# Performance work log

Hardware: AMD Instinct MI355X
Metric: run time of the kernel (lower is better)

## Reference

```python
import jax, jax.numpy as jnp
import numpy as np

B, CIN, COUT, H, W = 16, 64, 64, 128, 128
MH, MW = 32, 32  # retained Fourier modes


def setup_inputs() -> dict:
    key = jax.random.key(0)
    k1, k2, k3 = jax.random.split(key, 3)
    scale = 1.0 / (CIN * COUT)  # 'auto' scale in the torch module
    x = jax.random.normal(k1, (B, CIN, H, W), dtype=jnp.float32)
    # packed complex weight: dim0 = (real, imag), dim1 = corner (top=0, bottom=1)
    weight = scale * jax.random.normal(k2, (2, 2, CIN, COUT, MH, MW), dtype=jnp.float32)
    bias = scale * jax.random.normal(k3, (COUT, 1, 1), dtype=jnp.float32)
    return {"x": x, "weight": weight, "bias": bias, "super_res": 1}


def reference(x, weight, bias, super_res):
    b, ci, h, w = x.shape
    # rfft2 over the last two spatial dims (norm='backward' is default)
    xf = jnp.fft.rfft2(x.astype(jnp.float32), norm="backward")  # [b, ci, h, w//2+1] c64
    wc = (weight[0] + 1j * weight[1]).astype(jnp.complex64)  # [2, ci, co, mh, mw]
    # low-frequency corner contractions: bixy,ioxy->boxy
    top = jnp.einsum("bixy,ioxy->boxy", xf[:, :, :MH, :MW], wc[0])
    bot = jnp.einsum("bixy,ioxy->boxy", xf[:, :, h - MH:, :MW], wc[1])
    out_fft = jnp.zeros((b, COUT, h, w // 2 + 1), dtype=jnp.complex64)
    out_fft = out_fft.at[:, :, :MH, :MW:super_res].set(top)
    out_fft = out_fft.at[:, :, h - MH:, :MW:super_res].set(bot)
    out_size = (int(h * super_res), int(w * super_res))
    y = jnp.fft.irfft2(out_fft, s=out_size, norm="backward").astype(x.dtype)
    return y + bias  # bias [co,1,1] broadcasts over spatial dims
```

## Files before the change

### kernel.cpp

```cpp
#include <hip/hip_runtime.h>


__device__ __forceinline__ void build_tab(float* tabs) {
    int t = threadIdx.x;
    if (t < 128) {
        float ang = (float)t * 0.049087385212340517f;
        float s, c;
        sincosf(ang, &s, &c);
        tabs[t] = c;
        tabs[129 + t] = s;
    }
}

__global__ __launch_bounds__(256) void kAB(const float* __restrict__ x,
                                           float* __restrict__ XF) {
    __shared__ float tabs[258];
    __shared__ __align__(16) float smem[8704];
    build_tab(tabs);
    __syncthreads();
    int t = threadIdx.x;
    size_t bc = blockIdx.x;
    float* Twid = smem;
    float* xeo  = smem + 4096;
    #pragma unroll
    for (int i = 0; i < 16; ++i) {
        int e = t + i * 256;
        int w = e >> 6, q = e & 63, kx = q >> 1;
        int idx = (w * kx) & 127;
        Twid[e] = (q & 1) ? -tabs[129 + idx] : tabs[idx];
    }
    const float* xb = x + bc * 16384;
    int th = t & 31;
    int tq = t >> 5;
    int q0 = tq * 8;
    int wl4 = (t & 3) * 4;
    int hb  = t >> 2;
    float4 rlo0, rhi0, rlo1, rhi1;
    auto loadR = [&](int ph) {
        rlo0 = *(const float4*)(xb + hb * 128 + ph * 16 + wl4);
        rhi0 = *(const float4*)(xb + hb * 128 + ph * 16 + wl4 + 64);
        rlo1 = *(const float4*)(xb + (64 + hb) * 128 + ph * 16 + wl4);
        rhi1 = *(const float4*)(xb + (64 + hb) * 128 + ph * 16 + wl4 + 64);
    };
    auto writeR = [&]() {
        int h0 = hb, h1 = 64 + hb;
        *(float2*)(&xeo[(wl4+0)*260 + 2*h0]) = make_float2(rlo0.x+rhi0.x, rlo0.x-rhi0.x);
        *(float2*)(&xeo[(wl4+1)*260 + 2*h0]) = make_float2(rlo0.y+rhi0.y, rlo0.y-rhi0.y);
        *(float2*)(&xeo[(wl4+2)*260 + 2*h0]) = make_float2(rlo0.z+rhi0.z, rlo0.z-rhi0.z);
        *(float2*)(&xeo[(wl4+3)*260 + 2*h0]) = make_float2(rlo0.w+rhi0.w, rlo0.w-rhi0.w);
        *(float2*)(&xeo[(wl4+0)*260 + 2*h1]) = make_float2(rlo1.x+rhi1.x, rlo1.x-rhi1.x);
        *(float2*)(&xeo[(wl4+1)*260 + 2*h1]) = make_float2(rlo1.y+rhi1.y, rlo1.y-rhi1.y);
        *(float2*)(&xeo[(wl4+2)*260 + 2*h1]) = make_float2(rlo1.z+rhi1.z, rlo1.z-rhi1.z);
        *(float2*)(&xeo[(wl4+3)*260 + 2*h1]) = make_float2(rlo1.w+rhi1.w, rlo1.w-rhi1.w);
    };
    loadR(0);
    writeR();
    float4 acc[8];
    #pragma unroll
    for (int j = 0; j < 8; ++j) acc[j] = make_float4(0.f, 0.f, 0.f, 0.f);
    __syncthreads();
    for (int ph = 0; ph < 4; ++ph) {
        if (ph < 3) loadR(ph + 1);
        #pragma unroll 4
        for (int wl = 0; wl < 16; ++wl) {
            int w = ph * 16 + wl;
            const float* xr = &xeo[wl * 260 + 4 * th];
            float4 d0  = *(const float4*)(xr);
            float4 d1  = *(const float4*)(xr + 128);
            float4 tw0 = *(const float4*)(&Twid[w * 64 + q0]);
            float4 tw1 = *(const float4*)(&Twid[w * 64 + q0 + 4]);
            acc[0].x = fmaf(d0.x, tw0.x, acc[0].x); acc[0].y = fmaf(d0.x, tw0.y, acc[0].y);
            acc[0].z = fmaf(d0.y, tw0.z, acc[0].z); acc[0].w = fmaf(d0.y, tw0.w, acc[0].w);
            acc[1].x = fmaf(d0.x, tw1.x, acc[1].x); acc[1].y = fmaf(d0.x, tw1.y, acc[1].y);
            acc[1].z = fmaf(d0.y, tw1.z, acc[1].z); acc[1].w = fmaf(d0.y, tw1.w, acc[1].w);
            acc[2].x = fmaf(d0.z, tw0.x, acc[2].x); acc[2].y = fmaf(d0.z, tw0.y, acc[2].y);
            acc[2].z = fmaf(d0.w, tw0.z, acc[2].z); acc[2].w = fmaf(d0.w, tw0.w, acc[2].w);
            acc[3].x = fmaf(d0.z, tw1.x, acc[3].x); acc[3].y = fmaf(d0.z, tw1.y, acc[3].y);
            acc[3].z = fmaf(d0.w, tw1.z, acc[3].z); acc[3].w = fmaf(d0.w, tw1.w, acc[3].w);
            acc[4].x = fmaf(d1.x, tw0.x, acc[4].x); acc[4].y = fmaf(d1.x, tw0.y, acc[4].y);
            acc[4].z = fmaf(d1.y, tw0.z, acc[4].z); acc[4].w = fmaf(d1.y, tw0.w, acc[4].w);
            acc[5].x = fmaf(d1.x, tw1.x, acc[5].x); acc[5].y = fmaf(d1.x, tw1.y, acc[5].y);
            acc[5].z = fmaf(d1.y, tw1.z, acc[5].z); acc[5].w = fmaf(d1.y, tw1.w, acc[5].w);
            acc[6].x = fmaf(d1.z, tw0.x, acc[6].x); acc[6].y = fmaf(d1.z, tw0.y, acc[6].y);
            acc[6].z = fmaf(d1.w, tw0.z, acc[6].z); acc[6].w = fmaf(d1.w, tw0.w, acc[6].w);
            acc[7].x = fmaf(d1.z, tw1.x, acc[7].x); acc[7].y = fmaf(d1.z, tw1.y, acc[7].y);
            acc[7].z = fmaf(d1.w, tw1.z, acc[7].z); acc[7].w = fmaf(d1.w, tw1.w, acc[7].w);
        }
        __syncthreads();
        if (ph < 3) {
            writeR();
            __syncthreads();
        }
    }
    float* Af = smem;
    {
        int base = th * 68 + q0;
        *(float4*)(&Af[base])          = make_float4(acc[0].x+acc[4].x, acc[0].y+acc[4].y, acc[0].z+acc[4].z, acc[0].w+acc[4].w);
        *(float4*)(&Af[base + 4])      = make_float4(acc[1].x+acc[5].x, acc[1].y+acc[5].y, acc[1].z+acc[5].z, acc[1].w+acc[5].w);
        *(float4*)(&Af[2176 + base])   = make_float4(acc[0].x-acc[4].x, acc[0].y-acc[4].y, acc[0].z-acc[4].z, acc[0].w-acc[4].w);
        *(float4*)(&Af[2176 + base+4]) = make_float4(acc[1].x-acc[5].x, acc[1].y-acc[5].y, acc[1].z-acc[5].z, acc[1].w-acc[5].w);
        *(float4*)(&Af[4352 + base])   = make_float4(acc[2].x+acc[6].x, acc[2].y+acc[6].y, acc[2].z+acc[6].z, acc[2].w+acc[6].w);
        *(float4*)(&Af[4352 + base+4]) = make_float4(acc[3].x+acc[7].x, acc[3].y+acc[7].y, acc[3].z+acc[7].z, acc[3].w+acc[7].w);
        *(float4*)(&Af[6528 + base])   = make_float4(acc[2].x-acc[6].x, acc[2].y-acc[6].y, acc[2].z-acc[6].z, acc[2].w-acc[6].w);
        *(float4*)(&Af[6528 + base+4]) = make_float4(acc[3].x-acc[7].x, acc[3].y-acc[7].y, acc[3].z-acc[7].z, acc[3].w-acc[7].w);
    }
    __syncthreads();
    {
        int k = t & 31, kxg = t >> 5;
        int kx0 = kxg * 4;
        int sig = k & 1;
        const float* pe = Af + sig * 2176;
        const float* po = Af + 4352 + sig * 2176;
        int a2 = (2 * k) & 127;
        float ca = tabs[a2], sa = tabs[129 + a2];
        float ce = 1.f, se = 0.f;
        float co_ = tabs[k], so_ = tabs[129 + k];
        float4 P1 = {0,0,0,0}, P2 = {0,0,0,0}, P3 = {0,0,0,0}, P4 = {0,0,0,0};
        for (int m = 0; m < 32; ++m) {
            float4 ae01 = *(const float4*)(pe + m * 68 + 2 * kx0);
            float4 ae23 = *(const float4*)(pe + m * 68 + 2 * kx0 + 4);
            float4 ao01 = *(const float4*)(po + m * 68 + 2 * kx0);
            float4 ao23 = *(const float4*)(po + m * 68 + 2 * kx0 + 4);
            P1.x = fmaf(ae01.x, ce, P1.x); P1.x = fmaf(ao01.x, co_, P1.x);
            P2.x = fmaf(ae01.y, se, P2.x); P2.x = fmaf(ao01.y, so_, P2.x);
            P3.x = fmaf(ae01.y, ce, P3.x); P3.x = fmaf(ao01.y, co_, P3.x);
            P4.x = fmaf(ae01.x, se, P4.x); P4.x = fmaf(ao01.x, so_, P4.x);
            P1.y = fmaf(ae01.z, ce, P1.y); P1.y = fmaf(ao01.z, co_, P1.y);
            P2.y = fmaf(ae01.w, se, P2.y); P2.y = fmaf(ao01.w, so_, P2.y);
            P3.y = fmaf(ae01.w, ce, P3.y); P3.y = fmaf(ao01.w, co_, P3.y);
            P4.y = fmaf(ae01.z, se, P4.y); P4.y = fmaf(ao01.z, so_, P4.y);
            P1.z = fmaf(ae23.x, ce, P1.z); P1.z = fmaf(ao23.x, co_, P1.z);
            P2.z = fmaf(ae23.y, se, P2.z); P2.z = fmaf(ao23.y, so_, P2.z);
            P3.z = fmaf(ae23.y, ce, P3.z); P3.z = fmaf(ao23.y, co_, P3.z);
            P4.z = fmaf(ae23.x, se, P4.z); P4.z = fmaf(ao23.x, so_, P4.z);
            P1.w = fmaf(ae23.z, ce, P1.w); P1.w = fmaf(ao23.z, co_, P1.w);
            P2.w = fmaf(ae23.w, se, P2.w); P2.w = fmaf(ao23.w, so_, P2.w);
            P3.w = fmaf(ae23.w, ce, P3.w); P3.w = fmaf(ao23.w, co_, P3.w);
            P4.w = fmaf(ae23.z, se, P4.w); P4.w = fmaf(ao23.z, so_, P4.w);
            float t1 = se * sa, t2 = ce * sa;
            float cen = fmaf(ce, ca, -t1);
            float sen = fmaf(se, ca, t2);
            ce = cen; se = sen;
            float t3 = so_ * sa, t4 = co_ * sa;
            float con = fmaf(co_, ca, -t3);
            float son = fmaf(so_, ca, t4);
            co_ = con; so_ = son;
        }
        float* xfb = XF + bc * 4096;
        *(float4*)(xfb + (k * 32 + kx0) * 2) =
            make_float4(P1.x + P2.x, P3.x - P4.x, P1.y + P2.y, P3.y - P4.y);
        *(float4*)(xfb + (k * 32 + kx0) * 2 + 4) =
            make_float4(P1.z + P2.z, P3.z - P4.z, P1.w + P2.w, P3.w - P4.w);
        if (k) {
            *(float4*)(xfb + ((64 - k) * 32 + kx0) * 2) =
                make_float4(P1.x - P2.x, P3.x + P4.x, P1.y - P2.y, P3.y + P4.y);
            *(float4*)(xfb + ((64 - k) * 32 + kx0) * 2 + 4) =
                make_float4(P1.z - P2.z, P3.z + P4.z, P1.w - P2.w, P3.w + P4.w);
        }
        if (t < 32) {
            int kx = t;
            float re = 0.f, im = 0.f;
            #pragma unroll 8
            for (int m = 0; m < 32; ++m) {
                float2 aep = *(const float2*)(&Af[       m * 68 + 2 * kx]);
                float2 aop = *(const float2*)(&Af[4352 + m * 68 + 2 * kx]);
                float sg = (m & 1) ? -1.f : 1.f;
                re = fmaf(sg, aep.x - aop.y, re);
                im = fmaf(sg, aep.y + aop.x, im);
            }
            xfb[(32 * 32 + kx) * 2]     = re;
            xfb[(32 * 32 + kx) * 2 + 1] = im;
        }
    }
}

__global__ __launch_bounds__(256, 4) void kC(const float* __restrict__ XF,
                                             const float* __restrict__ Wgt,
                                             float* __restrict__ YF0,
                                             float* __restrict__ YF1) {
    __shared__ float2 Xs[2048];
    int t = threadIdx.x;
    int bid = blockIdx.x;
    int cih = bid & 1;
    int mxh = (bid >> 1) & 1;
    int cot = (bid >> 2) & 3;
    int my  = (bid >> 4) & 31;
    int c   = bid >> 9;
    int co0 = cot * 16;
    int slotbase = (c * 32 + my) * 32 + mxh * 16;
    int mx = t & 15;
    int co_l = t >> 4;
    int co = co0 + co_l;
    int ci0 = cih * 32;
    float2 acc[16];
    #pragma unroll
    for (int i = 0; i < 16; ++i) acc[i] = make_float2(0.f, 0.f);
    const float* wp = Wgt + (size_t)c * 4194304 + (size_t)my * 32 + mxh * 16 + mx
                          + ((size_t)(ci0 * 64) + co) * 1024;
    float2 rw0[8], rw1[8], rw2[8], rw3[8], rx[8];
    auto loadW = [&](int cc, float2* rw) {
        #pragma unroll
        for (int j = 0; j < 8; ++j) {
            size_t off = (size_t)(cc * 8 + j) * 65536;
            rw[j].x = wp[off];
            rw[j].y = wp[off + 8388608];
        }
    };
    auto loadX = [&](int cc) {
        #pragma unroll
        for (int s = 0; s < 8; ++s) {
            int e = t + s * 256;
            int emx = e & 15, eb = (e >> 4) & 15, eci = e >> 8;
            int ci = ci0 + cc * 8 + eci;
            rx[s] = *(const float2*)(XF + ((size_t)(eb * 64 + ci) * 2048 + slotbase + emx) * 2);
        }
    };
    auto writeX = [&]() {
        #pragma unroll
        for (int s = 0; s < 8; ++s) Xs[t + s * 256] = rx[s];
    };
#define KC_COMPUTE(RW)                                                       \
    {                                                                        \
        _Pragma("unroll")                                                    \
        for (int j = 0; j < 8; ++j) {                                        \
            float2 w = RW[j];                                                \
            _Pragma("unroll")                                                \
            for (int b = 0; b < 16; ++b) {                                   \
                float2 xv = Xs[(j * 16 + b) * 16 + mx];                      \
                acc[b].x = fmaf(xv.x, w.x, acc[b].x);                        \
                acc[b].x = fmaf(-xv.y, w.y, acc[b].x);                       \
                acc[b].y = fmaf(xv.x, w.y, acc[b].y);                        \
                acc[b].y = fmaf(xv.y, w.x, acc[b].y);                        \
            }                                                                \
        }                                                                    \
    }
    loadX(0);
    loadW(0, rw0); loadW(1, rw1); loadW(2, rw2);
    writeX();
    __syncthreads();
    loadX(1);
    loadW(3, rw3);
    KC_COMPUTE(rw0);
    __syncthreads();
    writeX(); __syncthreads();
    loadX(2);
    KC_COMPUTE(rw1);
    __syncthreads();
    writeX(); __syncthreads();
    loadX(3);
    KC_COMPUTE(rw2);
    __syncthreads();
    writeX(); __syncthreads();
    KC_COMPUTE(rw3);
#undef KC_COMPUTE
    float* YF = cih ? YF1 : YF0;
    #pragma unroll
    for (int b = 0; b < 16; ++b) {
        *(float2*)(YF + ((size_t)(b * 64 + co) * 2048 + slotbase + mx) * 2) = acc[b];
    }
}

__global__ __launch_bounds__(256) void kDE(const float* __restrict__ YF0,
                                           const float* __restrict__ YF1,
                                           const float* __restrict__ bias,
                                           float* __restrict__ out) {
    __shared__ float tabs[258];
    __shared__ __align__(16) float Ts[4096];
    __shared__ __align__(16) float U[8448];
    build_tab(tabs);
    __syncthreads();
    int t = threadIdx.x;
    size_t bo = blockIdx.x;
    const float inv = 6.103515625e-05f;
    #pragma unroll
    for (int i = 0; i < 16; ++i) {
        int e = t + i * 256;
        int q = e >> 6, w = e & 63;
        int k = q >> 1;
        int idx = (k * w) & 127;
        float val;
        if (q == 0)      val = inv;
        else if (q == 1) val = 0.f;
        else if (q & 1)  val = -2.f * inv * tabs[129 + idx];
        else             val =  2.f * inv * tabs[idx];
        Ts[e] = val;
    }
    float* Qs = U;
    float* Rs = U + 2112;
    const float* y0 = YF0 + bo * 4096;
    const float* y1 = YF1 + bo * 4096;
    for (int u = t; u < 528; u += 256) {
        int k = u >> 4, kxf = (u & 15) * 4;
        float4 a0 = *(const float4*)(y0 + k * 64 + kxf);
        float4 a1 = *(const float4*)(y1 + k * 64 + kxf);
        float4 a = make_float4(a0.x+a1.x, a0.y+a1.y, a0.z+a1.z, a0.w+a1.w);
        float4 Q, R;
        if (k == 0) { Q = a; R = make_float4(0.f, 0.f, 0.f, 0.f); }
        else if (k == 32) { Q = a; R = make_float4(-a.x, -a.y, -a.z, -a.w); }
        else {
            float4 b0 = *(const float4*)(y0 + (64 - k) * 64 + kxf);
            float4 b1 = *(const float4*)(y1 + (64 - k) * 64 + kxf);
            float4 bb = make_float4(b0.x+b1.x, b0.y+b1.y, b0.z+b1.z, b0.w+b1.w);
            Q = make_float4(a.x+bb.x, a.y+bb.y, a.z+bb.z, a.w+bb.w);
            R = make_float4(a.x-bb.x, a.y-bb.y, a.z-bb.z, a.w-bb.w);
        }
        *(float4*)(&Qs[k * 64 + kxf]) = Q;
        *(float4*)(&Rs[k * 64 + kxf]) = R;
    }
    __syncthreads();
    int hh = t >> 2;
    int kx0 = (t & 3) * 8;
    float4 Ee0 = {0,0,0,0}, Ee1 = {0,0,0,0}, Ee2 = {0,0,0,0}, Ee3 = {0,0,0,0};
    float4 Eo0 = {0,0,0,0}, Eo1 = {0,0,0,0}, Eo2 = {0,0,0,0}, Eo3 = {0,0,0,0};
    int idx = 0;
#define KD_BODY(E0, E1, E2, E3, kk)                                          \
    {                                                                        \
        float c = tabs[idx], s = tabs[129 + idx];                            \
        const float4* Qp = (const float4*)(&Qs[(kk) * 64 + kx0 * 2]);        \
        const float4* Rp = (const float4*)(&Rs[(kk) * 64 + kx0 * 2]);        \
        float4 Qv, Rv;                                                       \
        Qv = Qp[0]; Rv = Rp[0];                                              \
        E0.x = fmaf(c, Qv.x, E0.x); E0.x = fmaf(-s, Rv.y, E0.x);             \
        E0.y = fmaf(c, Qv.y, E0.y); E0.y = fmaf(s, Rv.x, E0.y);              \
        E0.z = fmaf(c, Qv.z, E0.z); E0.z = fmaf(-s, Rv.w, E0.z);             \
        E0.w = fmaf(c, Qv.w, E0.w); E0.w = fmaf(s, Rv.z, E0.w);              \
        Qv = Qp[1]; Rv = Rp[1];                                              \
        E1.x = fmaf(c, Qv.x, E1.x); E1.x = fmaf(-s, Rv.y, E1.x);             \
        E1.y = fmaf(c, Qv.y, E1.y); E1.y = fmaf(s, Rv.x, E1.y);              \
        E1.z = fmaf(c, Qv.z, E1.z); E1.z = fmaf(-s, Rv.w, E1.z);             \
        E1.w = fmaf(c, Qv.w, E1.w); E1.w = fmaf(s, Rv.z, E1.w);              \
        Qv = Qp[2]; Rv = Rp[2];                                              \
        E2.x = fmaf(c, Qv.x, E2.x); E2.x = fmaf(-s, Rv.y, E2.x);             \
        E2.y = fmaf(c, Qv.y, E2.y); E2.y = fmaf(s, Rv.x, E2.y);              \
        E2.z = fmaf(c, Qv.z, E2.z); E2.z = fmaf(-s, Rv.w, E2.z);             \
        E2.w = fmaf(c, Qv.w, E2.w); E2.w = fmaf(s, Rv.z, E2.w);              \
        Qv = Qp[3]; Rv = Rp[3];                                              \
        E3.x = fmaf(c, Qv.x, E3.x); E3.x = fmaf(-s, Rv.y, E3.x);             \
        E3.y = fmaf(c, Qv.y, E3.y); E3.y = fmaf(s, Rv.x, E3.y);              \
        E3.z = fmaf(c, Qv.z, E3.z); E3.z = fmaf(-s, Rv.w, E3.z);             \
        E3.w = fmaf(c, Qv.w, E3.w); E3.w = fmaf(s, Rv.z, E3.w);              \
        idx = (idx + hh) & 127;                                              \
    }
    for (int u = 0; u < 16; ++u) {
        KD_BODY(Ee0, Ee1, Ee2, Ee3, 2 * u);
        KD_BODY(Eo0, Eo1, Eo2, Eo3, 2 * u + 1);
    }
    KD_BODY(Ee0, Ee1, Ee2, Ee3, 32);
#undef KD_BODY
    __syncthreads();
    float* Zt = U;
    {
        float* zr = &Zt[(2 * kx0) * 132 + hh];
        float* zs = zr + 64;
        zr[0*132]  = Ee0.x + Eo0.x;  zs[0*132]  = Ee0.x - Eo0.x;
        zr[1*132]  = Ee0.y + Eo0.y;  zs[1*132]  = Ee0.y - Eo0.y;
        zr[2*132]  = Ee0.z + Eo0.z;  zs[2*132]  = Ee0.z - Eo0.z;
        zr[3*132]  = Ee0.w + Eo0.w;  zs[3*132]  = Ee0.w - Eo0.w;
        zr[4*132]  = Ee1.x + Eo1.x;  zs[4*132]  = Ee1.x - Eo1.x;
        zr[5*132]  = Ee1.y + Eo1.y;  zs[5*132]  = Ee1.y - Eo1.y;
        zr[6*132]  = Ee1.z + Eo1.z;  zs[6*132]  = Ee1.z - Eo1.z;
        zr[7*132]  = Ee1.w + Eo1.w;  zs[7*132]  = Ee1.w - Eo1.w;
        zr[8*132]  = Ee2.x + Eo2.x;  zs[8*132]  = Ee2.x - Eo2.x;
        zr[9*132]  = Ee2.y + Eo2.y;  zs[9*132]  = Ee2.y - Eo2.y;
        zr[10*132] = Ee2.z + Eo2.z;  zs[10*132] = Ee2.z - Eo2.z;
        zr[11*132] = Ee2.w + Eo2.w;  zs[11*132] = Ee2.w - Eo2.w;
        zr[12*132] = Ee3.x + Eo3.x;  zs[12*132] = Ee3.x - Eo3.x;
        zr[13*132] = Ee3.y + Eo3.y;  zs[13*132] = Ee3.y - Eo3.y;
        zr[14*132] = Ee3.z + Eo3.z;  zs[14*132] = Ee3.z - Eo3.z;
        zr[15*132] = Ee3.w + Eo3.w;  zs[15*132] = Ee3.w - Eo3.w;
    }
    __syncthreads();
    int w0 = (t & 31) * 2;
    int h0 = (t >> 5) * 16;
    float2 We[16], Wo[16];
    #pragma unroll
    for (int j = 0; j < 16; ++j) { We[j] = make_float2(0.f, 0.f); Wo[j] = make_float2(0.f, 0.f); }
#define KE_K(E, K)                                                            \
    {                                                                         \
        const float4* zpe = (const float4*)(&Zt[(2*(K)) * 132 + h0]);         \
        const float4* zpo = (const float4*)(&Zt[(2*(K)+1) * 132 + h0]);       \
        float2 twe = *(const float2*)(&Ts[(2*(K)) * 64 + w0]);                \
        float2 two = *(const float2*)(&Ts[(2*(K)+1) * 64 + w0]);              \
        float4 e0 = zpe[0], e1 = zpe[1], e2 = zpe[2], e3 = zpe[3];            \
        float4 o0 = zpo[0], o1 = zpo[1], o2 = zpo[2], o3 = zpo[3];            \
        E[0].x  = fmaf(e0.x, twe.x, E[0].x);  E[0].x  = fmaf(o0.x, two.x, E[0].x);   \
        E[0].y  = fmaf(e0.x, twe.y, E[0].y);  E[0].y  = fmaf(o0.x, two.y, E[0].y);   \
        E[1].x  = fmaf(e0.y, twe.x, E[1].x);  E[1].x  = fmaf(o0.y, two.x, E[1].x);   \
        E[1].y  = fmaf(e0.y, twe.y, E[1].y);  E[1].y  = fmaf(o0.y, two.y, E[1].y);   \
        E[2].x  = fmaf(e0.z, twe.x, E[2].x);  E[2].x  = fmaf(o0.z, two.x, E[2].x);   \
        E[2].y  = fmaf(e0.z, twe.y, E[2].y);  E[2].y  = fmaf(o0.z, two.y, E[2].y);   \
        E[3].x  = fmaf(e0.w, twe.x, E[3].x);  E[3].x  = fmaf(o0.w, two.x, E[3].x);   \
        E[3].y  = fmaf(e0.w, twe.y, E[3].y);  E[3].y  = fmaf(o0.w, two.y, E[3].y);   \
        E[4].x  = fmaf(e1.x, twe.x, E[4].x);  E[4].x  = fmaf(o1.x, two.x, E[4].x);   \
        E[4].y  = fmaf(e1.x, twe.y, E[4].y);  E[4].y  = fmaf(o1.x, two.y, E[4].y);   \
        E[5].x  = fmaf(e1.y, twe.x, E[5].x);  E[5].x  = fmaf(o1.y, two.x, E[5].x);   \
        E[5].y  = fmaf(e1.y, twe.y, E[5].y);  E[5].y  = fmaf(o1.y, two.y, E[5].y);   \
        E[6].x  = fmaf(e1.z, twe.x, E[6].x);  E[6].x  = fmaf(o1.z, two.x, E[6].x);   \
        E[6].y  = fmaf(e1.z, twe.y, E[6].y);  E[6].y  = fmaf(o1.z, two.y, E[6].y);   \
        E[7].x  = fmaf(e1.w, twe.x, E[7].x);  E[7].x  = fmaf(o1.w, two.x, E[7].x);   \
        E[7].y  = fmaf(e1.w, twe.y, E[7].y);  E[7].y  = fmaf(o1.w, two.y, E[7].y);   \
        E[8].x  = fmaf(e2.x, twe.x, E[8].x);  E[8].x  = fmaf(o2.x, two.x, E[8].x);   \
        E[8].y  = fmaf(e2.x, twe.y, E[8].y);  E[8].y  = fmaf(o2.x, two.y, E[8].y);   \
        E[9].x  = fmaf(e2.y, twe.x, E[9].x);  E[9].x  = fmaf(o2.y, two.x, E[9].x);   \
        E[9].y  = fmaf(e2.y, twe.y, E[9].y);  E[9].y  = fmaf(o2.y, two.y, E[9].y);   \
        E[10].x = fmaf(e2.z, twe.x, E[10].x); E[10].x = fmaf(o2.z, two.x, E[10].x);  \
        E[10].y = fmaf(e2.z, twe.y, E[10].y); E[10].y = fmaf(o2.z, two.y, E[10].y);  \
        E[11].x = fmaf(e2.w, twe.x, E[11].x); E[11].x = fmaf(o2.w, two.x, E[11].x);  \
        E[11].y = fmaf(e2.w, twe.y, E[11].y); E[11].y = fmaf(o2.w, two.y, E[11].y);  \
        E[12].x = fmaf(e3.x, twe.x, E[12].x); E[12].x = fmaf(o3.x, two.x, E[12].x);  \
        E[12].y = fmaf(e3.x, twe.y, E[12].y); E[12].y = fmaf(o3.x, two.y, E[12].y);  \
        E[13].x = fmaf(e3.y, twe.x, E[13].x); E[13].x = fmaf(o3.y, two.x, E[13].x);  \
        E[13].y = fmaf(e3.y, twe.y, E[13].y); E[13].y = fmaf(o3.y, two.y, E[13].y);  \
        E[14].x = fmaf(e3.z, twe.x, E[14].x); E[14].x = fmaf(o3.z, two.x, E[14].x);  \
        E[14].y = fmaf(e3.z, twe.y, E[14].y); E[14].y = fmaf(o3.z, two.y, E[14].y);  \
        E[15].x = fmaf(e3.w, twe.x, E[15].x); E[15].x = fmaf(o3.w, two.x, E[15].x);  \
        E[15].y = fmaf(e3.w, twe.y, E[15].y); E[15].y = fmaf(o3.w, two.y, E[15].y);  \
    }
    #pragma unroll 2
    for (int u = 0; u < 16; ++u) {
        KE_K(We, 2 * u);
        KE_K(Wo, 2 * u + 1);
    }
#undef KE_K
    float bv = bias[(int)(bo & 63)];
    float* ob = out + ((size_t)(bo * 128 + h0)) * 128;
    #pragma unroll
    for (int j = 0; j < 16; ++j) {
        float2 lo = make_float2(We[j].x + Wo[j].x + bv, We[j].y + Wo[j].y + bv);
        float2 hi = make_float2(We[j].x - Wo[j].x + bv, We[j].y - Wo[j].y + bv);
        *(float2*)(ob + (size_t)j * 128 + w0)      = lo;
        *(float2*)(ob + (size_t)j * 128 + w0 + 64) = hi;
    }
}

extern "C" void kernel_launch(void* const* d_in, const int* in_sizes, int n_in,
                              void* d_out, int out_size, void* d_ws, size_t ws_size,
                              hipStream_t stream) {
    (void)in_sizes; (void)n_in; (void)out_size; (void)ws_size;
    const float* x    = (const float*)d_in[0];
    const float* wgt  = (const float*)d_in[1];
    const float* bias = (const float*)d_in[2];
    float* outp   = (float*)d_out;
    char* ws = (char*)d_ws;
    float* bufXF  = (float*)(ws + (48u << 20));
    float* bufYF0 = (float*)(ws);
    float* bufYF1 = (float*)(ws + (16u << 20));
    hipLaunchKernelGGL(kAB, dim3(1024), dim3(256), 0, stream, x, bufXF);
    hipLaunchKernelGGL(kC, dim3(1024), dim3(256), 0, stream, bufXF, wgt, bufYF0, bufYF1);
    hipLaunchKernelGGL(kDE, dim3(1024), dim3(256), 0, stream, bufYF0, bufYF1, bias, outp);
}
```

Baseline: 116.9 us.

## Split kC work over batch halves and double-buffer weight registers

The spectral contraction kernel now assigns each block 8 output channels and splits the 16-batch dimension across two thread halves, so each thread keeps 8 accumulators instead of 16. The grid doubles to 2048 blocks. Weight prefetch moves from four register buffers to two ping-pong buffers that are reloaded after each compute stage. This lowers register pressure and adds parallelism, at the cost of loading each X tile in twice as many blocks and exposing more of the weight-load latency.

```diff
diff --git a/kernel.cpp b/kernel.cpp
--- a/kernel.cpp
+++ b/kernel.cpp
@@ -183,21 +183,22 @@
     int bid = blockIdx.x;
     int cih = bid & 1;
     int mxh = (bid >> 1) & 1;
-    int cot = (bid >> 2) & 3;
-    int my  = (bid >> 4) & 31;
-    int c   = bid >> 9;
-    int co0 = cot * 16;
+    int cot = (bid >> 2) & 7;
+    int my  = (bid >> 5) & 31;
+    int c   = bid >> 10;
+    int co0 = cot * 8;
     int slotbase = (c * 32 + my) * 32 + mxh * 16;
-    int mx = t & 15;
-    int co_l = t >> 4;
+    int mx   = t & 15;
+    int co_l = (t >> 4) & 7;
+    int bh   = t >> 7;
     int co = co0 + co_l;
     int ci0 = cih * 32;
-    float2 acc[16];
-    #pragma unroll
-    for (int i = 0; i < 16; ++i) acc[i] = make_float2(0.f, 0.f);
+    float2 acc[8];
+    #pragma unroll
+    for (int i = 0; i < 8; ++i) acc[i] = make_float2(0.f, 0.f);
     const float* wp = Wgt + (size_t)c * 4194304 + (size_t)my * 32 + mxh * 16 + mx
                           + ((size_t)(ci0 * 64) + co) * 1024;
-    float2 rw0[8], rw1[8], rw2[8], rw3[8], rx[8];
+    float2 rwA[8], rwB[8], rx[8];
     auto loadW = [&](int cc, float2* rw) {
         #pragma unroll
         for (int j = 0; j < 8; ++j) {
@@ -225,38 +226,39 @@
         for (int j = 0; j < 8; ++j) {                                        \
             float2 w = RW[j];                                                \
             _Pragma("unroll")                                                \
-            for (int b = 0; b < 16; ++b) {                                   \
-                float2 xv = Xs[(j * 16 + b) * 16 + mx];                      \
-                acc[b].x = fmaf(xv.x, w.x, acc[b].x);                        \
-                acc[b].x = fmaf(-xv.y, w.y, acc[b].x);                       \
-                acc[b].y = fmaf(xv.x, w.y, acc[b].y);                        \
-                acc[b].y = fmaf(xv.y, w.x, acc[b].y);                        \
+            for (int bb = 0; bb < 8; ++bb) {                                 \
+                float2 xv = Xs[(j * 16 + bh * 8 + bb) * 16 + mx];            \
+                acc[bb].x = fmaf(xv.x, w.x, acc[bb].x);                      \
+                acc[bb].x = fmaf(-xv.y, w.y, acc[bb].x);                     \
+                acc[bb].y = fmaf(xv.x, w.y, acc[bb].y);                      \
+                acc[bb].y = fmaf(xv.y, w.x, acc[bb].y);                      \
             }                                                                \
         }                                                                    \
     }
-    loadX(0);
-    loadW(0, rw0); loadW(1, rw1); loadW(2, rw2);
+    loadX(0); loadW(0, rwA); loadW(1, rwB);
     writeX();
     __syncthreads();
     loadX(1);
-    loadW(3, rw3);
-    KC_COMPUTE(rw0);
+    KC_COMPUTE(rwA);
+    loadW(2, rwA);
     __syncthreads();
     writeX(); __syncthreads();
     loadX(2);
-    KC_COMPUTE(rw1);
+    KC_COMPUTE(rwB);
+    loadW(3, rwB);
     __syncthreads();
     writeX(); __syncthreads();
     loadX(3);
-    KC_COMPUTE(rw2);
+    KC_COMPUTE(rwA);
     __syncthreads();
     writeX(); __syncthreads();
-    KC_COMPUTE(rw3);
+    KC_COMPUTE(rwB);
 #undef KC_COMPUTE
     float* YF = cih ? YF1 : YF0;
     #pragma unroll
-    for (int b = 0; b < 16; ++b) {
-        *(float2*)(YF + ((size_t)(b * 64 + co) * 2048 + slotbase + mx) * 2) = acc[b];
+    for (int bb = 0; bb < 8; ++bb) {
+        int b = bh * 8 + bb;
+        *(float2*)(YF + ((size_t)(b * 64 + co) * 2048 + slotbase + mx) * 2) = acc[bb];
     }
 }
 
@@ -446,6 +448,6 @@
     float* bufYF0 = (float*)(ws);
     float* bufYF1 = (float*)(ws + (16u << 20));
     hipLaunchKernelGGL(kAB, dim3(1024), dim3(256), 0, stream, x, bufXF);
-    hipLaunchKernelGGL(kC, dim3(1024), dim3(256), 0, stream, bufXF, wgt, bufYF0, bufYF1);
+    hipLaunchKernelGGL(kC, dim3(2048), dim3(256), 0, stream, bufXF, wgt, bufYF0, bufYF1);
     hipLaunchKernelGGL(kDE, dim3(1024), dim3(256), 0, stream, bufYF0, bufYF1, bias, outp);
 }
```

Result: no change. 117.1 us (+0.1%).
